# Kernel tuning notes

Measured on AMD Instinct MI355X. Metric: run time of the kernel, lower is better.

The kernel has to match this reference:

```python
import jax, jax.numpy as jnp
import numpy as np

VOCAB_PRI = 100000
VOCAB_SEC = 100000
EMBED_DIM = 64


def setup_inputs() -> dict:
    key = jax.random.key(0)
    k1, k2, k3, k4 = jax.random.split(key, 4)
    inputs_pri = jax.random.randint(k1, (4096, 200), 0, VOCAB_PRI, dtype=jnp.int64 if jax.config.jax_enable_x64 else jnp.int32)
    inputs_sec = jax.random.randint(k2, (4096, 200), 0, VOCAB_SEC, dtype=jnp.int64 if jax.config.jax_enable_x64 else jnp.int32)
    initrange = 0.01
    emb_pri = jax.random.uniform(k3, (VOCAB_PRI, EMBED_DIM), jnp.float32, -initrange, initrange)
    emb_sec = jax.random.uniform(k4, (VOCAB_SEC, EMBED_DIM), jnp.float32, -initrange, initrange)
    return {"inputs_pri": inputs_pri, "inputs_sec": inputs_sec,
            "emb_pri": emb_pri, "emb_sec": emb_sec}


def _embed_sum(table, idx):
    # gather [B, S, D] then sum over sentence dim -> [B, D]
    # (equivalent to cAdd's per-token accumulation / EmbeddingBag(sum))
    return jnp.sum(table[idx], axis=1)


def reference(inputs_pri, inputs_sec, emb_pri, emb_sec):
    out_pri = _embed_sum(emb_pri, inputs_pri)  # [B, D]
    out_sec = _embed_sum(emb_sec, inputs_sec)  # [B, D]
    return out_pri, out_sec
```

## Files before the change

### kernel.cpp

```cpp
#include <hip/hip_runtime.h>
#include <hip/hip_bf16.h>


#define BB 4096
#define SS 200
#define DD 64
#define VOCAB 100000

__global__ __launch_bounds__(256) void convert_bf16_2(
    const float* __restrict__ src0, const float* __restrict__ src1,
    uint2* __restrict__ dst0, uint2* __restrict__ dst1)
{
    const unsigned NT = (unsigned)VOCAB * DD / 4;
    unsigned g = blockIdx.x * 256u + threadIdx.x;
    const float* __restrict__ src = src0;
    uint2* __restrict__ dst = dst0;
    if (g >= NT) { g -= NT; src = src1; dst = dst1; }
    const float4 v = ((const float4*)src)[g];
    const unsigned u0 = __bfloat16_as_ushort(__float2bfloat16(v.x));
    const unsigned u1 = __bfloat16_as_ushort(__float2bfloat16(v.y));
    const unsigned u2 = __bfloat16_as_ushort(__float2bfloat16(v.z));
    const unsigned u3 = __bfloat16_as_ushort(__float2bfloat16(v.w));
    uint2 o;
    o.x = u0 | (u1 << 16);
    o.y = u2 | (u3 << 16);
    dst[g] = o;
}

__global__ __launch_bounds__(256) void embed_sum_bf16_x4(
    const int* __restrict__ idx_pri, const int* __restrict__ idx_sec,
    const uint4* __restrict__ tbl_pri, const uint4* __restrict__ tbl_sec,
    float* __restrict__ out)
{
    __shared__ int sidx[4][SS];

    const int tid  = (int)threadIdx.x;
    const int w    = tid >> 6;
    const int lane = tid & 63;
    const int blk  = (int)blockIdx.x;
    const int t    = blk >> 10;
    const int bi   = blk & 1023;

    const int*   __restrict__ idx = t ? idx_sec : idx_pri;
    const uint4* __restrict__ tbl = t ? tbl_sec : tbl_pri;

    const int* ib = idx + (size_t)bi * 4 * SS;
    if (tid < (4 * SS) / 4) {
        const int4 v = ((const int4*)ib)[tid];
        int* s = &sidx[0][0];
        s[tid * 4 + 0] = v.x;
        s[tid * 4 + 1] = v.y;
        s[tid * 4 + 2] = v.z;
        s[tid * 4 + 3] = v.w;
    }
    __syncthreads();

    const int g  = lane >> 3;
    const int l8 = lane & 7;

    float a0 = 0.f, a1 = 0.f, a2 = 0.f, a3 = 0.f;
    float a4 = 0.f, a5 = 0.f, a6 = 0.f, a7 = 0.f;

    #pragma unroll 5
    for (int k = 0; k < 25; ++k) {
        const int i = sidx[w][8 * k + g];
        const uint4 v = tbl[(unsigned)i * 8u + l8];
        a0 += __uint_as_float(v.x << 16);
        a1 += __uint_as_float(v.x & 0xffff0000u);
        a2 += __uint_as_float(v.y << 16);
        a3 += __uint_as_float(v.y & 0xffff0000u);
        a4 += __uint_as_float(v.z << 16);
        a5 += __uint_as_float(v.z & 0xffff0000u);
        a6 += __uint_as_float(v.w << 16);
        a7 += __uint_as_float(v.w & 0xffff0000u);
    }

    a0 += __shfl_down(a0, 32); a1 += __shfl_down(a1, 32);
    a2 += __shfl_down(a2, 32); a3 += __shfl_down(a3, 32);
    a4 += __shfl_down(a4, 32); a5 += __shfl_down(a5, 32);
    a6 += __shfl_down(a6, 32); a7 += __shfl_down(a7, 32);
    a0 += __shfl_down(a0, 16); a1 += __shfl_down(a1, 16);
    a2 += __shfl_down(a2, 16); a3 += __shfl_down(a3, 16);
    a4 += __shfl_down(a4, 16); a5 += __shfl_down(a5, 16);
    a6 += __shfl_down(a6, 16); a7 += __shfl_down(a7, 16);
    a0 += __shfl_down(a0, 8);  a1 += __shfl_down(a1, 8);
    a2 += __shfl_down(a2, 8);  a3 += __shfl_down(a3, 8);
    a4 += __shfl_down(a4, 8);  a5 += __shfl_down(a5, 8);
    a6 += __shfl_down(a6, 8);  a7 += __shfl_down(a7, 8);

    if (g == 0) {
        const int b = bi * 4 + w;
        float* outp = out + (size_t)t * BB * DD + (size_t)b * DD + l8 * 8;
        float4 lo; lo.x = a0; lo.y = a1; lo.z = a2; lo.w = a3;
        float4 hi; hi.x = a4; hi.y = a5; hi.z = a6; hi.w = a7;
        ((float4*)outp)[0] = lo;
        ((float4*)outp)[1] = hi;
    }
}

__global__ __launch_bounds__(256) void bilingual_embed_sum(
    const int* __restrict__ idx_pri,
    const int* __restrict__ idx_sec,
    const float* __restrict__ emb_pri,
    const float* __restrict__ emb_sec,
    float* __restrict__ out)
{
    __shared__ int sidx[4][SS];
    const int w    = (int)(threadIdx.x >> 6);
    const int lane = (int)(threadIdx.x & 63);
    const int wave = (int)(blockIdx.x * 4 + w);
    const int table = wave >> 12;
    const int b     = wave & (BB - 1);

    const int*   idx = table ? idx_sec : idx_pri;
    const float* emb = table ? emb_sec : emb_pri;
    float* outp = out + (size_t)table * BB * DD + (size_t)b * DD;

    const int* row_idx = idx + b * SS;
    if (lane < SS / 4) {
        const int4 v = ((const int4*)row_idx)[lane];
        sidx[w][lane * 4 + 0] = v.x;
        sidx[w][lane * 4 + 1] = v.y;
        sidx[w][lane * 4 + 2] = v.z;
        sidx[w][lane * 4 + 3] = v.w;
    }
    __syncthreads();

    const int q   = lane >> 4;
    const int l16 = lane & 15;
    float4 acc = make_float4(0.f, 0.f, 0.f, 0.f);

    #pragma unroll 10
    for (int s0 = 0; s0 < SS; s0 += 4) {
        const int i = sidx[w][s0 + q];
        const float4 v = ((const float4*)(emb + (size_t)i * DD))[l16];
        acc.x += v.x; acc.y += v.y; acc.z += v.z; acc.w += v.w;
    }

    acc.x += __shfl_down(acc.x, 32);
    acc.y += __shfl_down(acc.y, 32);
    acc.z += __shfl_down(acc.z, 32);
    acc.w += __shfl_down(acc.w, 32);
    acc.x += __shfl_down(acc.x, 16);
    acc.y += __shfl_down(acc.y, 16);
    acc.z += __shfl_down(acc.z, 16);
    acc.w += __shfl_down(acc.w, 16);

    if (lane < 16) ((float4*)outp)[l16] = acc;
}

extern "C" void kernel_launch(void* const* d_in, const int* in_sizes, int n_in,
                              void* d_out, int out_size, void* d_ws, size_t ws_size,
                              hipStream_t stream) {
    const int*   idx_pri = (const int*)d_in[0];
    const int*   idx_sec = (const int*)d_in[1];
    const float* emb_pri = (const float*)d_in[2];
    const float* emb_sec = (const float*)d_in[3];
    float* out = (float*)d_out;

    const size_t tbl_u2 = (size_t)VOCAB * DD / 4;
    const size_t ws_need = tbl_u2 * 8 * 2;

    if (ws_size >= ws_need) {
        uint2* t0 = (uint2*)d_ws;
        uint2* t1 = t0 + tbl_u2;
        const int conv_grid   = (2 * VOCAB * DD / 4) / 256;
        const int gather_grid = 2 * (BB / 4);

        convert_bf16_2<<<conv_grid, 256, 0, stream>>>(emb_pri, emb_sec, t0, t1);
        embed_sum_bf16_x4<<<gather_grid, 256, 0, stream>>>(
            idx_pri, idx_sec, (const uint4*)t0, (const uint4*)t1, out);
    } else {
        bilingual_embed_sum<<<(2 * BB) / 4, 256, 0, stream>>>(
            idx_pri, idx_sec, emb_pri, emb_sec, out);
    }
}
```

Measured before the change: 119.1 us.

## Fuse bf16 table conversion and gather into one cooperative kernel with grid sync

Replaces the separate conversion and gather launches with a single cooperative kernel. It first grid-strides over both tables converting them to bf16, then does a grid-wide sync, then gathers with 1024 blocks of which each wave handles two batch rows. This removes one launch and the gap between kernels, and doubles the loads in flight per wave. The cost is a grid sync, fewer total waves, and a fallback to the old two-kernel path if the cooperative launch fails.

Result: slower. 238.5 us (+100.2%).

```diff
diff --git a/kernel.cpp b/kernel.cpp
--- a/kernel.cpp
+++ b/kernel.cpp
@@ -1,5 +1,8 @@
 #include <hip/hip_runtime.h>
 #include <hip/hip_bf16.h>
+#include <hip/hip_cooperative_groups.h>
+
+namespace cg = cooperative_groups;
 
 
 #define BB 4096
@@ -7,16 +10,9 @@
 #define DD 64
 #define VOCAB 100000
 
-__global__ __launch_bounds__(256) void convert_bf16_2(
-    const float* __restrict__ src0, const float* __restrict__ src1,
-    uint2* __restrict__ dst0, uint2* __restrict__ dst1)
-{
-    const unsigned NT = (unsigned)VOCAB * DD / 4;
-    unsigned g = blockIdx.x * 256u + threadIdx.x;
-    const float* __restrict__ src = src0;
-    uint2* __restrict__ dst = dst0;
-    if (g >= NT) { g -= NT; src = src1; dst = dst1; }
-    const float4 v = ((const float4*)src)[g];
+#define GATHER_BLOCKS 1024
+
+__device__ __forceinline__ uint2 pack_bf16x4(const float4 v) {
     const unsigned u0 = __bfloat16_as_ushort(__float2bfloat16(v.x));
     const unsigned u1 = __bfloat16_as_ushort(__float2bfloat16(v.y));
     const unsigned u2 = __bfloat16_as_ushort(__float2bfloat16(v.z));
@@ -24,7 +20,123 @@
     uint2 o;
     o.x = u0 | (u1 << 16);
     o.y = u2 | (u3 << 16);
-    dst[g] = o;
+    return o;
+}
+
+__global__ __launch_bounds__(256) void fused_convert_gather(
+    const int* __restrict__ idx_pri, const int* __restrict__ idx_sec,
+    const float* __restrict__ emb_pri, const float* __restrict__ emb_sec,
+    uint2* __restrict__ t0, uint2* __restrict__ t1,
+    float* __restrict__ out)
+{
+    {
+        const unsigned NT    = (unsigned)VOCAB * DD / 4;
+        const unsigned total = 2u * NT;
+        const unsigned step  = gridDim.x * 256u;
+        for (unsigned g = blockIdx.x * 256u + threadIdx.x; g < total; g += step) {
+            const float* __restrict__ src;
+            uint2* __restrict__ dst;
+            unsigned o;
+            if (g < NT) { src = emb_pri; dst = t0; o = g; }
+            else        { src = emb_sec; dst = t1; o = g - NT; }
+            dst[o] = pack_bf16x4(((const float4*)src)[o]);
+        }
+    }
+
+    cg::this_grid().sync();
+
+    __shared__ int sidx[8][SS];
+
+    const int tid = (int)threadIdx.x;
+    const int blk = (int)blockIdx.x;
+    const int t   = blk >> 9;
+    const int bi  = blk & 511;
+
+    const int*   __restrict__ idx = t ? idx_sec : idx_pri;
+    const uint4* __restrict__ tbl = (const uint4*)(t ? t1 : t0);
+
+    const int* ib = idx + (size_t)bi * 8 * SS;
+    #pragma unroll
+    for (int j = tid; j < (8 * SS) / 4; j += 256) {
+        const int4 v = ((const int4*)ib)[j];
+        int* s = &sidx[0][0];
+        s[j * 4 + 0] = v.x;
+        s[j * 4 + 1] = v.y;
+        s[j * 4 + 2] = v.z;
+        s[j * 4 + 3] = v.w;
+    }
+    __syncthreads();
+
+    const int w    = tid >> 6;
+    const int lane = tid & 63;
+    const int g    = lane >> 3;
+    const int l8   = lane & 7;
+
+    float aA[8];
+    float aB[8];
+    #pragma unroll
+    for (int r = 0; r < 8; ++r) { aA[r] = 0.f; aB[r] = 0.f; }
+
+    #pragma unroll 5
+    for (int k = 0; k < 25; ++k) {
+        const int iA = sidx[w][8 * k + g];
+        const int iB = sidx[w + 4][8 * k + g];
+        const uint4 vA = tbl[(unsigned)iA * 8u + l8];
+        const uint4 vB = tbl[(unsigned)iB * 8u + l8];
+        aA[0] += __uint_as_float(vA.x << 16);
+        aA[1] += __uint_as_float(vA.x & 0xffff0000u);
+        aA[2] += __uint_as_float(vA.y << 16);
+        aA[3] += __uint_as_float(vA.y & 0xffff0000u);
+        aA[4] += __uint_as_float(vA.z << 16);
+        aA[5] += __uint_as_float(vA.z & 0xffff0000u);
+        aA[6] += __uint_as_float(vA.w << 16);
+        aA[7] += __uint_as_float(vA.w & 0xffff0000u);
+        aB[0] += __uint_as_float(vB.x << 16);
+        aB[1] += __uint_as_float(vB.x & 0xffff0000u);
+        aB[2] += __uint_as_float(vB.y << 16);
+        aB[3] += __uint_as_float(vB.y & 0xffff0000u);
+        aB[4] += __uint_as_float(vB.z << 16);
+        aB[5] += __uint_as_float(vB.z & 0xffff0000u);
+        aB[6] += __uint_as_float(vB.w << 16);
+        aB[7] += __uint_as_float(vB.w & 0xffff0000u);
+    }
+
+    #pragma unroll
+    for (int sh = 32; sh >= 8; sh >>= 1) {
+        #pragma unroll
+        for (int r = 0; r < 8; ++r) {
+            aA[r] += __shfl_down(aA[r], sh);
+            aB[r] += __shfl_down(aB[r], sh);
+        }
+    }
+
+    if (g == 0) {
+        const int bA = bi * 8 + w;
+        const int bB = bi * 8 + 4 + w;
+        float* oA = out + (size_t)t * BB * DD + (size_t)bA * DD + l8 * 8;
+        float* oB = out + (size_t)t * BB * DD + (size_t)bB * DD + l8 * 8;
+        float4 lo, hi;
+        lo.x = aA[0]; lo.y = aA[1]; lo.z = aA[2]; lo.w = aA[3];
+        hi.x = aA[4]; hi.y = aA[5]; hi.z = aA[6]; hi.w = aA[7];
+        ((float4*)oA)[0] = lo;
+        ((float4*)oA)[1] = hi;
+        lo.x = aB[0]; lo.y = aB[1]; lo.z = aB[2]; lo.w = aB[3];
+        hi.x = aB[4]; hi.y = aB[5]; hi.z = aB[6]; hi.w = aB[7];
+        ((float4*)oB)[0] = lo;
+        ((float4*)oB)[1] = hi;
+    }
+}
+
+__global__ __launch_bounds__(256) void convert_bf16_2(
+    const float* __restrict__ src0, const float* __restrict__ src1,
+    uint2* __restrict__ dst0, uint2* __restrict__ dst1)
+{
+    const unsigned NT = (unsigned)VOCAB * DD / 4;
+    unsigned g = blockIdx.x * 256u + threadIdx.x;
+    const float* __restrict__ src = src0;
+    uint2* __restrict__ dst = dst0;
+    if (g >= NT) { g -= NT; src = src1; dst = dst1; }
+    dst[g] = pack_bf16x4(((const float4*)src)[g]);
 }
 
 __global__ __launch_bounds__(256) void embed_sum_bf16_x4(
@@ -58,41 +170,36 @@
     const int g  = lane >> 3;
     const int l8 = lane & 7;
 
-    float a0 = 0.f, a1 = 0.f, a2 = 0.f, a3 = 0.f;
-    float a4 = 0.f, a5 = 0.f, a6 = 0.f, a7 = 0.f;
+    float a[8];
+    #pragma unroll
+    for (int r = 0; r < 8; ++r) a[r] = 0.f;
 
     #pragma unroll 5
     for (int k = 0; k < 25; ++k) {
         const int i = sidx[w][8 * k + g];
         const uint4 v = tbl[(unsigned)i * 8u + l8];
-        a0 += __uint_as_float(v.x << 16);
-        a1 += __uint_as_float(v.x & 0xffff0000u);
-        a2 += __uint_as_float(v.y << 16);
-        a3 += __uint_as_float(v.y & 0xffff0000u);
-        a4 += __uint_as_float(v.z << 16);
-        a5 += __uint_as_float(v.z & 0xffff0000u);
-        a6 += __uint_as_float(v.w << 16);
-        a7 += __uint_as_float(v.w & 0xffff0000u);
-    }
-
-    a0 += __shfl_down(a0, 32); a1 += __shfl_down(a1, 32);
-    a2 += __shfl_down(a2, 32); a3 += __shfl_down(a3, 32);
-    a4 += __shfl_down(a4, 32); a5 += __shfl_down(a5, 32);
-    a6 += __shfl_down(a6, 32); a7 += __shfl_down(a7, 32);
-    a0 += __shfl_down(a0, 16); a1 += __shfl_down(a1, 16);
-    a2 += __shfl_down(a2, 16); a3 += __shfl_down(a3, 16);
-    a4 += __shfl_down(a4, 16); a5 += __shfl_down(a5, 16);
-    a6 += __shfl_down(a6, 16); a7 += __shfl_down(a7, 16);
-    a0 += __shfl_down(a0, 8);  a1 += __shfl_down(a1, 8);
-    a2 += __shfl_down(a2, 8);  a3 += __shfl_down(a3, 8);
-    a4 += __shfl_down(a4, 8);  a5 += __shfl_down(a5, 8);
-    a6 += __shfl_down(a6, 8);  a7 += __shfl_down(a7, 8);
+        a[0] += __uint_as_float(v.x << 16);
+        a[1] += __uint_as_float(v.x & 0xffff0000u);
+        a[2] += __uint_as_float(v.y << 16);
+        a[3] += __uint_as_float(v.y & 0xffff0000u);
+        a[4] += __uint_as_float(v.z << 16);
+        a[5] += __uint_as_float(v.z & 0xffff0000u);
+        a[6] += __uint_as_float(v.w << 16);
+        a[7] += __uint_as_float(v.w & 0xffff0000u);
+    }
+
+    #pragma unroll
+    for (int sh = 32; sh >= 8; sh >>= 1) {
+        #pragma unroll
+        for (int r = 0; r < 8; ++r) a[r] += __shfl_down(a[r], sh);
+    }
 
     if (g == 0) {
         const int b = bi * 4 + w;
         float* outp = out + (size_t)t * BB * DD + (size_t)b * DD + l8 * 8;
-        float4 lo; lo.x = a0; lo.y = a1; lo.z = a2; lo.w = a3;
-        float4 hi; hi.x = a4; hi.y = a5; hi.z = a6; hi.w = a7;
+        float4 lo, hi;
+        lo.x = a[0]; lo.y = a[1]; lo.z = a[2]; lo.w = a[3];
+        hi.x = a[4]; hi.y = a[5]; hi.z = a[6]; hi.w = a[7];
         ((float4*)outp)[0] = lo;
         ((float4*)outp)[1] = hi;
     }
@@ -152,8 +259,8 @@
 extern "C" void kernel_launch(void* const* d_in, const int* in_sizes, int n_in,
                               void* d_out, int out_size, void* d_ws, size_t ws_size,
                               hipStream_t stream) {
-    const int*   idx_pri = (const int*)d_in[0];
-    const int*   idx_sec = (const int*)d_in[1];
+    const int* idx_pri = (const int*)d_in[0];
+    const int* idx_sec = (const int*)d_in[1];
     const float* emb_pri = (const float*)d_in[2];
     const float* emb_sec = (const float*)d_in[3];
     float* out = (float*)d_out;
@@ -164,12 +271,22 @@
     if (ws_size >= ws_need) {
         uint2* t0 = (uint2*)d_ws;
         uint2* t1 = t0 + tbl_u2;
-        const int conv_grid   = (2 * VOCAB * DD / 4) / 256;
-        const int gather_grid = 2 * (BB / 4);
-
-        convert_bf16_2<<<conv_grid, 256, 0, stream>>>(emb_pri, emb_sec, t0, t1);
-        embed_sum_bf16_x4<<<gather_grid, 256, 0, stream>>>(
-            idx_pri, idx_sec, (const uint4*)t0, (const uint4*)t1, out);
+
+        void* args[] = { (void*)&idx_pri, (void*)&idx_sec,
+                         (void*)&emb_pri, (void*)&emb_sec,
+                         (void*)&t0, (void*)&t1, (void*)&out };
+        const hipError_t e = hipLaunchCooperativeKernel(
+            (const void*)fused_convert_gather,
+            dim3(GATHER_BLOCKS), dim3(256), args, 0, stream);
+
+        if (e != hipSuccess) {
+            const int conv_grid   = (2 * VOCAB * DD / 4) / 256;
+            const int gather_grid = 2 * (BB / 4);
+            convert_bf16_2<<<conv_grid, 256, 0, stream>>>(emb_pri, emb_sec,
+                                                          t0, t1);
+            embed_sum_bf16_x4<<<gather_grid, 256, 0, stream>>>(
+                idx_pri, idx_sec, (const uint4*)t0, (const uint4*)t1, out);
+        }
     } else {
         bilingual_embed_sum<<<(2 * BB) / 4, 256, 0, stream>>>(
             idx_pri, idx_sec, emb_pri, emb_sec, out);
```
